# Optimization experiments

Hardware: AMD Instinct MI355X
Metric: run time of the kernel (lower is better)

Reference implementation:

```python
import jax, jax.numpy as jnp
import numpy as np
import math

B, T, H, NH, BLOCK = 2, 2048, 1024, 16, 2048
HS = H // NH  # 64, even as required by RoPE


def make_rope_cache(hs, block):
    # positions t = 1..block (note: source starts at 1, not 0)
    t = np.arange(1, block + 1, dtype=np.float32)[:, None]          # (block, 1)
    i = np.arange(1, hs // 2 + 1, dtype=np.float32)[None, :]        # (1, hs/2)
    theta = (1.0 / 10000.0) ** (2.0 * (i - 1.0) / hs)               # (1, hs/2)
    ang = t * theta                                                  # (block, hs/2)
    return jnp.asarray(np.stack([np.cos(ang), np.sin(ang)], axis=-1))  # (block, hs/2, 2)


def setup_inputs() -> dict:
    key = jax.random.key(0)
    ks = jax.random.split(key, 10)
    s = 0.02
    x = jax.random.normal(ks[0], (B, T, H), jnp.float32)
    masks = jax.random.randint(ks[1], (B, T), 0, 2, jnp.int32)  # 1 = padding token
    Wq = jax.random.normal(ks[2], (H, H), jnp.float32) * s
    bq = jnp.zeros((H,), jnp.float32)
    Wk = jax.random.normal(ks[3], (H, H), jnp.float32) * s
    bk = jnp.zeros((H,), jnp.float32)
    Wv = jax.random.normal(ks[4], (H, H), jnp.float32) * s
    bv = jnp.zeros((H,), jnp.float32)
    Wo = jax.random.normal(ks[5], (H, H), jnp.float32) * s  # final_proj, no bias
    rope = make_rope_cache(HS, BLOCK)
    return {"x": x, "masks": masks, "Wq": Wq, "bq": bq, "Wk": Wk, "bk": bk,
            "Wv": Wv, "bv": bv, "Wo": Wo, "rope": rope}


def _apply_rope(x, cos, sin):
    # x: (B, nh, T, hs); cos/sin: (T, hs/2) broadcast over (B, nh)
    xe, xo = x[..., ::2], x[..., 1::2]
    real = cos * xe - sin * xo
    imag = sin * xe + cos * xo
    return jnp.stack([real, imag], axis=-1).reshape(x.shape)


def reference(x, masks, Wq, bq, Wk, bk, Wv, bv, Wo, rope):
    Bn, Tn, Hn = x.shape
    nh, hs = NH, Hn // NH

    def proj(W, b):
        # torch Linear: x @ W.T + b -> (B, nh, T, hs)
        return (x @ W.T + b).reshape(Bn, Tn, nh, hs).transpose(0, 2, 1, 3)

    Q, K, V = proj(Wq, bq), proj(Wk, bk), proj(Wv, bv)
    cos, sin = rope[:Tn, :, 0], rope[:Tn, :, 1]
    Q = _apply_rope(Q, cos, sin)
    K = _apply_rope(K, cos, sin)

    att = jnp.einsum('bhqd,bhkd->bhqk', Q, K) * (1.0 / math.sqrt(hs))
    causal = jnp.tril(jnp.ones((Tn, Tn), bool))
    att = jnp.where(causal[None, None, :, :], att, -1e10)          # causal mask
    att = jnp.where((masks == 1)[:, None, None, :], -1e10, att)   # padding mask on keys
    att = jax.nn.softmax(att, axis=-1)

    y = jnp.einsum('bhqk,bhkd->bhqd', att, V)
    y = y.transpose(0, 2, 1, 3).reshape(Bn, Tn, Hn)
    return y @ Wo.T  # final_proj has no bias
```

## Files before the change

### kernel.cpp

```cpp
#include <hip/hip_runtime.h>

typedef short short8 __attribute__((ext_vector_type(8)));
typedef float floatx4 __attribute__((ext_vector_type(4)));
typedef unsigned short u16;
typedef unsigned long long u64;

#define Tn 2048
#define Kdim 1024
#define QSCALE 0.18033688011112042f
#define FIXEDMAX 20.0f

__device__ inline u16 f2bf(float x) {
    union { float f; unsigned u; } c; c.f = x;
    unsigned u = c.u;
    u += 0x7fffu + ((u >> 16) & 1u);
    return (u16)(u >> 16);
}
__device__ inline float bf2f(u16 h) {
    union { unsigned u; float f; } c; c.u = ((unsigned)h) << 16;
    return c.f;
}
__device__ inline floatx4 mfma16(short8 a, short8 b, floatx4 c) {
    return __builtin_amdgcn_mfma_f32_16x16x32_bf16(a, b, c, 0, 0, 0);
}
__device__ inline void async16(const void* g, void* l) {
    __builtin_amdgcn_global_load_lds((const __attribute__((address_space(1))) void*)g,
                                     (__attribute__((address_space(3))) void*)l, 16, 0, 0);
}

__global__ __launch_bounds__(256) void cvt_all_k(
    const float* __restrict__ x, const float* __restrict__ wq, const float* __restrict__ wk,
    const float* __restrict__ wv, const float* __restrict__ wo, u16* __restrict__ dst,
    float4* __restrict__ vmz)
{
    int bx = blockIdx.x;
    if (bx >= 8192) {
        int j = threadIdx.x;
        float4 z = {0.f, 0.f, 0.f, 0.f};
        if (j < 512) vmz[j] = z;
        return;
    }
    int i = bx * 256 + threadIdx.x;
    const float* s; int off;
    if (i < 1048576) { s = x; off = i; }
    else {
        int j = i - 1048576; int seg = j >> 18; off = j & 262143;
        s = (seg == 0) ? wq : (seg == 1) ? wk : (seg == 2) ? wv : wo;
    }
    float4 v = ((const float4*)s)[off];
    u64 pk = (u64)f2bf(v.x) | ((u64)f2bf(v.y) << 16) | ((u64)f2bf(v.z) << 32) | ((u64)f2bf(v.w) << 48);
    ((u64*)dst)[i] = pk;
}

__global__ __launch_bounds__(256, 5) void gemm_qkv_k(
    const u16* __restrict__ A,
    const u16* __restrict__ W0, const u16* __restrict__ W1, const u16* __restrict__ W2,
    const float* __restrict__ b0, const float* __restrict__ b1, const float* __restrict__ b2,
    u16* o0, u16* o1, u16* o2,
    const float2* __restrict__ rope, float* __restrict__ vmean)
{
    int bid = blockIdx.x;
    int xcd = bid & 7, bi = bid >> 3;
    int z = bi >> 6;
    int r6 = bi & 63;
    int bx = (xcd & 1) * 8 + (r6 & 7);
    int by = (xcd >> 1) * 8 + (r6 >> 3);

    const u16* W = (z == 0) ? W0 : (z == 1 ? W1 : W2);
    const float* bias = (z == 0) ? b0 : (z == 1 ? b1 : b2);
    u16* outp = (z == 0) ? o0 : (z == 1 ? o1 : o2);

    __shared__ __align__(16) char lds[24576];
    int tid = threadIdx.x;
    int w = tid >> 6, lane = tid & 63, quad = lane >> 4, l15 = lane & 15;
    int m0 = by * 128, n0 = bx * 64;
    int wm = w * 32;

    floatx4 acc[2][4];
    floatx4 vzero = {0.f, 0.f, 0.f, 0.f};
#pragma unroll
    for (int i = 0; i < 2; ++i)
#pragma unroll
        for (int j = 0; j < 4; ++j) acc[i][j] = vzero;

    for (int k0 = 0; k0 < Kdim; k0 += 64) {
#pragma unroll
        for (int j = 0; j < 4; ++j) {
            int f = j * 256 + tid, r = f >> 3, c = (f & 7) ^ (r & 7);
            async16(A + (size_t)(m0 + r) * Kdim + k0 + c * 8, lds + j * 4096 + w * 1024);
        }
#pragma unroll
        for (int j = 0; j < 2; ++j) {
            int f = j * 256 + tid, r = f >> 3, c = (f & 7) ^ (r & 7);
            async16(W + (size_t)(n0 + r) * Kdim + k0 + c * 8, lds + 16384 + j * 4096 + w * 1024);
        }
        __syncthreads();
        short8 af[2][2];
#pragma unroll
        for (int mt = 0; mt < 2; ++mt) {
            int ra = wm + mt * 16 + l15;
            const char* pa = lds + ra * 128;
#pragma unroll
            for (int ks = 0; ks < 2; ++ks)
                af[mt][ks] = *(const short8*)(pa + (((ks * 4 + quad) ^ (ra & 7)) << 4));
        }
#pragma unroll
        for (int ks = 0; ks < 2; ++ks)
#pragma unroll
            for (int nt = 0; nt < 4; ++nt) {
                int rb = nt * 16 + l15;
                short8 bf = *(const short8*)(lds + 16384 + rb * 128 + (((ks * 4 + quad) ^ (rb & 7)) << 4));
                acc[0][nt] = mfma16(af[0][ks], bf, acc[0][nt]);
                acc[1][nt] = mfma16(af[1][ks], bf, acc[1][nt]);
            }
        __syncthreads();
    }

    int mbase = m0 + wm;
    if (z <= 1) {
        float osc = (z == 0) ? QSCALE : 1.0f;
#pragma unroll
        for (int nt = 0; nt < 4; ++nt) {
            int col = n0 + nt * 16 + l15;
            float bv = bias[col];
            int p = (col & 63) >> 1;
#pragma unroll
            for (int mt = 0; mt < 2; ++mt) {
                floatx4 a = acc[mt][nt];
#pragma unroll
                for (int r = 0; r < 4; ++r) {
                    int row = mbase + mt * 16 + quad * 4 + r;
                    float v = a[r] + bv;
                    float ov = __shfl_xor(v, 1, 64);
                    float2 cs = rope[(row & (Tn - 1)) * 32 + p];
                    float res = (cs.x * v + ((lane & 1) ? cs.y * ov : -cs.y * ov)) * osc;
                    float pres = __shfl_xor(res, 1, 64);
                    if (!(lane & 1)) {
                        unsigned pk = (unsigned)f2bf(res) | ((unsigned)f2bf(pres) << 16);
                        *(unsigned*)(outp + (size_t)row * 1024 + col) = pk;
                    }
                }
            }
        }
    } else {
#pragma unroll
        for (int nt = 0; nt < 4; ++nt) {
            int col = n0 + nt * 16 + l15;
            float bv = bias[col];
            float csum = 8.0f * bv;
#pragma unroll
            for (int mt = 0; mt < 2; ++mt) {
                floatx4 a = acc[mt][nt];
                int row0 = mbase + mt * 16 + quad * 4;
                int bb = row0 >> 11, t0 = row0 & (Tn - 1);
                u64 pk = (u64)f2bf(a[0] + bv) | ((u64)f2bf(a[1] + bv) << 16)
                       | ((u64)f2bf(a[2] + bv) << 32) | ((u64)f2bf(a[3] + bv) << 48);
                *(u64*)(outp + (size_t)(bb * 1024 + col) * Tn + t0) = pk;
                csum += a[0] + a[1] + a[2] + a[3];
            }
            csum += __shfl_xor(csum, 16, 64);
            csum += __shfl_xor(csum, 32, 64);
            if (quad == 0) {
                int bb = m0 >> 11;
                atomicAdd(&vmean[bb * 1024 + col], csum);
            }
        }
    }
}

__global__ __launch_bounds__(256, 5) void gemm_o_k(
    const u16* __restrict__ A, const u16* __restrict__ W, float* __restrict__ out)
{
    int bid = blockIdx.x;
    int xcd = bid & 7, bi = bid >> 3;
    int bx = (xcd & 1) * 8 + (bi & 7);
    int by = (xcd >> 1) * 8 + (bi >> 3);

    __shared__ __align__(16) char lds[24576];
    int tid = threadIdx.x;
    int w = tid >> 6, lane = tid & 63, quad = lane >> 4, l15 = lane & 15;
    int m0 = by * 128, n0 = bx * 64;
    int wm = w * 32;

    floatx4 acc[2][4];
    floatx4 vzero = {0.f, 0.f, 0.f, 0.f};
#pragma unroll
    for (int i = 0; i < 2; ++i)
#pragma unroll
        for (int j = 0; j < 4; ++j) acc[i][j] = vzero;

    for (int k0 = 0; k0 < Kdim; k0 += 64) {
#pragma unroll
        for (int j = 0; j < 4; ++j) {
            int f = j * 256 + tid, r = f >> 3, c = (f & 7) ^ (r & 7);
            async16(A + (size_t)(m0 + r) * Kdim + k0 + c * 8, lds + j * 4096 + w * 1024);
        }
#pragma unroll
        for (int j = 0; j < 2; ++j) {
            int f = j * 256 + tid, r = f >> 3, c = (f & 7) ^ (r & 7);
            async16(W + (size_t)(n0 + r) * Kdim + k0 + c * 8, lds + 16384 + j * 4096 + w * 1024);
        }
        __syncthreads();
        short8 af[2][2];
#pragma unroll
        for (int mt = 0; mt < 2; ++mt) {
            int ra = wm + mt * 16 + l15;
            const char* pa = lds + ra * 128;
#pragma unroll
            for (int ks = 0; ks < 2; ++ks)
                af[mt][ks] = *(const short8*)(pa + (((ks * 4 + quad) ^ (ra & 7)) << 4));
        }
#pragma unroll
        for (int ks = 0; ks < 2; ++ks)
#pragma unroll
            for (int nt = 0; nt < 4; ++nt) {
                int rb = nt * 16 + l15;
                short8 bf = *(const short8*)(lds + 16384 + rb * 128 + (((ks * 4 + quad) ^ (rb & 7)) << 4));
                acc[0][nt] = mfma16(af[0][ks], bf, acc[0][nt]);
                acc[1][nt] = mfma16(af[1][ks], bf, acc[1][nt]);
            }
        __syncthreads();
    }

#pragma unroll
    for (int nt = 0; nt < 4; ++nt) {
        int col = n0 + nt * 16 + l15;
#pragma unroll
        for (int mt = 0; mt < 2; ++mt) {
            floatx4 a = acc[mt][nt];
#pragma unroll
            for (int r = 0; r < 4; ++r) {
                int row = m0 + wm + mt * 16 + quad * 4 + r;
                out[(size_t)row * 1024 + col] = a[r];
            }
        }
    }
}

__global__ __launch_bounds__(256) void flash_k(
    const u16* __restrict__ Qb, const u16* __restrict__ Kb, const u16* __restrict__ Vt,
    const int* __restrict__ masks, const float* __restrict__ vmean, u16* __restrict__ Yb)
{
    int bid = blockIdx.x;
    int bh = (bid & 7) * 4 + ((bid >> 3) & 3);
    int idx = bid >> 5;
    int pg = idx >> 3, pr = idx & 7;
    int qt = (pg == 0) ? 31 - pr : (pg == 1) ? pr : (pg == 2) ? 23 - pr : 8 + pr;
    int b = bh >> 4, h = bh & 15;
    int tid = threadIdx.x, w = tid >> 6, lane = tid & 63, quad = lane >> 4, l15 = lane & 15;
    int sc = (lane & 7) ^ (lane >> 3);

    __shared__ __align__(16) u16 ldsK[2][64 * 64];
    __shared__ __align__(16) u16 ldsV[2][64 * 64];
    __shared__ __align__(16) u16 ldsP[4][16 * 64];

    int ktiles = qt + 1;
    unsigned blo = 0, bhi = 0;
    for (int j = 0; j < ktiles; ++j) {
        u64 mk = __ballot(masks[b * Tn + j * 64 + lane] != 0);
        if (lane == j) { blo = (unsigned)mk; bhi = (unsigned)(mk >> 32); }
    }

    auto stage = [&](int bb, int k0) {
#pragma unroll
        for (int j = 0; j < 2; ++j) {
            int row = j * 32 + w * 8 + (lane >> 3);
            const u16* gk = Kb + (size_t)(b * Tn + k0 + row) * 1024 + h * 64 + sc * 8;
            async16(gk, (char*)&ldsK[bb][0] + (j * 32 + w * 8) * 128);
            const u16* gv = Vt + (size_t)(b * 1024 + h * 64 + row) * Tn + k0 + sc * 8;
            async16(gv, (char*)&ldsV[bb][0] + (j * 32 + w * 8) * 128);
        }
    };
    floatx4 vzero = {0.f, 0.f, 0.f, 0.f};

    int q0 = qt * 64 + w * 16;
    short8 qf[2];
    {
        const u16* qp = Qb + (size_t)(b * Tn + q0 + l15) * 1024 + h * 64 + quad * 8;
        qf[0] = *(const short8*)qp;
        qf[1] = *(const short8*)(qp + 32);
    }
    floatx4 o[4];
    float lsum[4] = {0.f, 0.f, 0.f, 0.f};
#pragma unroll
    for (int i = 0; i < 4; ++i) o[i] = vzero;

    stage(0, 0);
    for (int kt = 0; kt < ktiles; ++kt) {
        int k0 = kt * 64;
        int bb = kt & 1;
        __syncthreads();

        short8 kf[4][2], vf[4][2];
#pragma unroll
        for (int f = 0; f < 4; ++f) {
            int key = f * 16 + l15;
            const char* kbase = (const char*)&ldsK[bb][0] + key * 128;
            const char* vbase = (const char*)&ldsV[bb][0] + key * 128;
#pragma unroll
            for (int ks = 0; ks < 2; ++ks) {
                int slot = ((quad + ks * 4) ^ (key & 7)) << 4;
                kf[f][ks] = *(const short8*)(kbase + slot);
                vf[f][ks] = *(const short8*)(vbase + slot);
            }
        }
        if (kt + 1 < ktiles) stage(bb ^ 1, k0 + 64);

        floatx4 s[4];
        __builtin_amdgcn_s_setprio(1);
#pragma unroll
        for (int f = 0; f < 4; ++f) {
            s[f] = mfma16(qf[0], kf[f][0], vzero);
            s[f] = mfma16(qf[1], kf[f][1], s[f]);
        }
        __builtin_amdgcn_s_setprio(0);

        unsigned mlo = __shfl(blo, kt, 64), mhi = __shfl(bhi, kt, 64);
        int mb[4];
        mb[0] = (mlo >> l15) & 1; mb[1] = (mlo >> (l15 + 16)) & 1;
        mb[2] = (mhi >> l15) & 1; mb[3] = (mhi >> (l15 + 16)) & 1;

        if (k0 + 63 <= q0) {
#pragma unroll
            for (int r = 0; r < 4; ++r) {
                float psum = 0.f;
#pragma unroll
                for (int f = 0; f < 4; ++f) {
                    float v = mb[f] ? -1e10f : s[f][r];
                    float p = __builtin_amdgcn_exp2f(v - FIXEDMAX);
                    psum += p;
                    unsigned u = __float_as_uint(p) + 0x8000u;
                    int row = quad * 4 + r, key = f * 16 + l15;
                    *((u16*)((char*)&ldsP[w][0] + row * 128 +
                             ((((key >> 3) ^ (row & 7))) << 4) + (key & 7) * 2)) = (u16)(u >> 16);
                }
                lsum[r] += psum;
            }
        } else {
#pragma unroll
            for (int r = 0; r < 4; ++r) {
                int lim = q0 + quad * 4 + r - k0;
                float psum = 0.f;
#pragma unroll
                for (int f = 0; f < 4; ++f) {
                    float v = (16 * f + l15 > lim || mb[f]) ? -1e10f : s[f][r];
                    float p = __builtin_amdgcn_exp2f(v - FIXEDMAX);
                    psum += p;
                    unsigned u = __float_as_uint(p) + 0x8000u;
                    int row = quad * 4 + r, key = f * 16 + l15;
                    *((u16*)((char*)&ldsP[w][0] + row * 128 +
                             ((((key >> 3) ^ (row & 7))) << 4) + (key & 7) * 2)) = (u16)(u >> 16);
                }
                lsum[r] += psum;
            }
        }
        __asm__ volatile("s_waitcnt lgkmcnt(0)" ::: "memory");
        short8 pf0 = *(const short8*)((const char*)&ldsP[w][0] + l15 * 128 + ((quad ^ (l15 & 7)) << 4));
        short8 pf1 = *(const short8*)((const char*)&ldsP[w][0] + l15 * 128 + (((quad + 4) ^ (l15 & 7)) << 4));
        __builtin_amdgcn_s_setprio(1);
#pragma unroll
        for (int nb = 0; nb < 4; ++nb) {
            o[nb] = mfma16(pf0, vf[nb][0], o[nb]);
            o[nb] = mfma16(pf1, vf[nb][1], o[nb]);
        }
        __builtin_amdgcn_s_setprio(0);
    }

#pragma unroll
    for (int r = 0; r < 4; ++r) {
        int qq = q0 + quad * 4 + r;
        float l = lsum[r];
#pragma unroll
        for (int off = 1; off < 16; off <<= 1) l += __shfl_xor(l, off, 64);
        bool degen = (l == 0.f);
        float linv = 1.0f / l;
#pragma unroll
        for (int nb = 0; nb < 4; ++nb) {
            int d = nb * 16 + l15;
            float val = degen ? vmean[b * 1024 + h * 64 + d] * (1.f / 2048.f) : o[nb][r] * linv;
            float pv = __shfl_xor(val, 1, 64);
            if (!(lane & 1)) {
                unsigned pk = (unsigned)f2bf(val) | ((unsigned)f2bf(pv) << 16);
                *(unsigned*)(Yb + (size_t)(b * Tn + qq) * 1024 + h * 64 + d) = pk;
            }
        }
    }
}

extern "C" void kernel_launch(void* const* d_in, const int* in_sizes, int n_in,
                              void* d_out, int out_size, void* d_ws, size_t ws_size,
                              hipStream_t stream) {
    const float* x  = (const float*)d_in[0];
    const int* masks = (const int*)d_in[1];
    const float* Wq = (const float*)d_in[2];
    const float* bq = (const float*)d_in[3];
    const float* Wk = (const float*)d_in[4];
    const float* bk = (const float*)d_in[5];
    const float* Wv = (const float*)d_in[6];
    const float* bv = (const float*)d_in[7];
    const float* Wo = (const float*)d_in[8];
    const float2* rope = (const float2*)d_in[9];
    float* out = (float*)d_out;

    char* ws = (char*)d_ws;
    u16* xb   = (u16*)(ws);
    u16* Wqb  = (u16*)(ws + (8  << 20));
    u16* Wkb  = (u16*)(ws + (10 << 20));
    u16* Wvb  = (u16*)(ws + (12 << 20));
    u16* Wob  = (u16*)(ws + (14 << 20));
    u16* Qb   = (u16*)(ws + (16 << 20));
    u16* Kb2  = (u16*)(ws + (24 << 20));
    u16* Vt   = (u16*)(ws + (32 << 20));
    u16* Yb   = (u16*)(ws + (40 << 20));
    float* vm = (float*)(ws + (48 << 20));

    cvt_all_k<<<8193, 256, 0, stream>>>(x, Wq, Wk, Wv, Wo, xb, (float4*)vm);

    gemm_qkv_k<<<1536, 256, 0, stream>>>(xb, Wqb, Wkb, Wvb, bq, bk, bv,
                                         Qb, Kb2, Vt, rope, vm);
    flash_k<<<1024, 256, 0, stream>>>(Qb, Kb2, Vt, masks, vm, Yb);
    gemm_o_k<<<512, 256, 0, stream>>>(Yb, Wob, out);
}
```

Before: 189.9 us.

## Compact non-padded keys/values so flash attention skips masked key tiles

Adds a prefix-sum kernel over the padding mask and scatters K and V rows into a compacted layout that holds only unmasked tokens, so flash attention iterates only over as many key tiles as there are valid keys up to the query tile. The combined causal/padding mask becomes a per-element comparison against the query's prefix count, folded into the MFMA accumulator init, and the per-tile ballot bitmask setup is removed. In exchange it adds an extra kernel launch, zeroing of the compacted K buffer, and scattered, uncoalesced V-transpose writes in the projection epilogue. With roughly half the tokens padded, the attention work should drop substantially.

```diff
diff --git a/kernel.cpp b/kernel.cpp
--- a/kernel.cpp
+++ b/kernel.cpp
@@ -31,13 +31,18 @@
 __global__ __launch_bounds__(256) void cvt_all_k(
     const float* __restrict__ x, const float* __restrict__ wq, const float* __restrict__ wk,
     const float* __restrict__ wv, const float* __restrict__ wo, u16* __restrict__ dst,
-    float4* __restrict__ vmz)
+    float4* __restrict__ vmz, float4* __restrict__ kvz)
 {
     int bx = blockIdx.x;
     if (bx >= 8192) {
-        int j = threadIdx.x;
+        int e = bx - 8192;
         float4 z = {0.f, 0.f, 0.f, 0.f};
-        if (j < 512) vmz[j] = z;
+        if (e == 0) {
+            vmz[threadIdx.x] = z;
+            vmz[threadIdx.x + 256] = z;
+        } else {
+            kvz[(e - 1) * 256 + threadIdx.x] = z;
+        }
         return;
     }
     int i = bx * 256 + threadIdx.x;
@@ -52,12 +57,31 @@
     ((u64*)dst)[i] = pk;
 }
 
+__global__ __launch_bounds__(1024) void compact_k(const int* __restrict__ masks, int* __restrict__ prefQ) {
+    int b = blockIdx.x, t = threadIdx.x;
+    __shared__ int tmp[1024];
+    int v0 = (masks[b * Tn + 2 * t] == 0);
+    int v1 = (masks[b * Tn + 2 * t + 1] == 0);
+    tmp[t] = v0 + v1;
+    __syncthreads();
+    for (int off = 1; off < 1024; off <<= 1) {
+        int v = (t >= off) ? tmp[t - off] : 0;
+        __syncthreads();
+        tmp[t] += v;
+        __syncthreads();
+    }
+    int incl = tmp[t];
+    prefQ[b * Tn + 2 * t] = incl - v1;
+    prefQ[b * Tn + 2 * t + 1] = incl;
+}
+
 __global__ __launch_bounds__(256, 5) void gemm_qkv_k(
     const u16* __restrict__ A,
     const u16* __restrict__ W0, const u16* __restrict__ W1, const u16* __restrict__ W2,
     const float* __restrict__ b0, const float* __restrict__ b1, const float* __restrict__ b2,
     u16* o0, u16* o1, u16* o2,
-    const float2* __restrict__ rope, float* __restrict__ vmean)
+    const float2* __restrict__ rope, float* __restrict__ vmean,
+    const int* __restrict__ masks, const int* __restrict__ prefQ)
 {
     int bid = blockIdx.x;
     int xcd = bid & 7, bi = bid >> 3;
@@ -68,7 +92,6 @@
 
     const u16* W = (z == 0) ? W0 : (z == 1 ? W1 : W2);
     const float* bias = (z == 0) ? b0 : (z == 1 ? b1 : b2);
-    u16* outp = (z == 0) ? o0 : (z == 1 ? o1 : o2);
 
     __shared__ __align__(16) char lds[24576];
     int tid = threadIdx.x;
@@ -127,9 +150,18 @@
 #pragma unroll
             for (int mt = 0; mt < 2; ++mt) {
                 floatx4 a = acc[mt][nt];
+                int row0 = mbase + mt * 16 + quad * 4;
+                int bb2 = row0 >> 11, tt0 = row0 & (Tn - 1);
+                int mka[4] = {0, 0, 0, 0}, pqa[4] = {0, 0, 0, 0};
+                if (z == 1) {
+                    int4 mk = *(const int4*)(masks + bb2 * Tn + tt0);
+                    int4 pq = *(const int4*)(prefQ + bb2 * Tn + tt0);
+                    mka[0] = mk.x; mka[1] = mk.y; mka[2] = mk.z; mka[3] = mk.w;
+                    pqa[0] = pq.x; pqa[1] = pq.y; pqa[2] = pq.z; pqa[3] = pq.w;
+                }
 #pragma unroll
                 for (int r = 0; r < 4; ++r) {
-                    int row = mbase + mt * 16 + quad * 4 + r;
+                    int row = row0 + r;
                     float v = a[r] + bv;
                     float ov = __shfl_xor(v, 1, 64);
                     float2 cs = rope[(row & (Tn - 1)) * 32 + p];
@@ -137,7 +169,12 @@
                     float pres = __shfl_xor(res, 1, 64);
                     if (!(lane & 1)) {
                         unsigned pk = (unsigned)f2bf(res) | ((unsigned)f2bf(pres) << 16);
-                        *(unsigned*)(outp + (size_t)row * 1024 + col) = pk;
+                        if (z == 0) {
+                            *(unsigned*)(o0 + (size_t)row * 1024 + col) = pk;
+                        } else if (mka[r] == 0) {
+                            int rowc = bb2 * Tn + pqa[r] - 1;
+                            *(unsigned*)(o1 + (size_t)rowc * 1024 + col) = pk;
+                        }
                     }
                 }
             }
@@ -152,10 +189,16 @@
             for (int mt = 0; mt < 2; ++mt) {
                 floatx4 a = acc[mt][nt];
                 int row0 = mbase + mt * 16 + quad * 4;
-                int bb = row0 >> 11, t0 = row0 & (Tn - 1);
-                u64 pk = (u64)f2bf(a[0] + bv) | ((u64)f2bf(a[1] + bv) << 16)
-                       | ((u64)f2bf(a[2] + bv) << 32) | ((u64)f2bf(a[3] + bv) << 48);
-                *(u64*)(outp + (size_t)(bb * 1024 + col) * Tn + t0) = pk;
+                int bb2 = row0 >> 11, t0 = row0 & (Tn - 1);
+                int4 mk = *(const int4*)(masks + bb2 * Tn + t0);
+                int4 pq = *(const int4*)(prefQ + bb2 * Tn + t0);
+                int mka[4] = {mk.x, mk.y, mk.z, mk.w};
+                int pqa[4] = {pq.x, pq.y, pq.z, pq.w};
+#pragma unroll
+                for (int i = 0; i < 4; ++i) {
+                    if (mka[i] == 0)
+                        o2[(size_t)(bb2 * 1024 + col) * Tn + pqa[i] - 1] = f2bf(a[i] + bv);
+                }
                 csum += a[0] + a[1] + a[2] + a[3];
             }
             csum += __shfl_xor(csum, 16, 64);
@@ -238,8 +281,8 @@
 }
 
 __global__ __launch_bounds__(256) void flash_k(
-    const u16* __restrict__ Qb, const u16* __restrict__ Kb, const u16* __restrict__ Vt,
-    const int* __restrict__ masks, const float* __restrict__ vmean, u16* __restrict__ Yb)
+    const u16* __restrict__ Qb, const u16* __restrict__ Kc, const u16* __restrict__ Vtc,
+    const int* __restrict__ prefQ, const float* __restrict__ vmean, u16* __restrict__ Yb)
 {
     int bid = blockIdx.x;
     int bh = (bid & 7) * 4 + ((bid >> 3) & 3);
@@ -254,26 +297,25 @@
     __shared__ __align__(16) u16 ldsV[2][64 * 64];
     __shared__ __align__(16) u16 ldsP[4][16 * 64];
 
-    int ktiles = qt + 1;
-    unsigned blo = 0, bhi = 0;
-    for (int j = 0; j < ktiles; ++j) {
-        u64 mk = __ballot(masks[b * Tn + j * 64 + lane] != 0);
-        if (lane == j) { blo = (unsigned)mk; bhi = (unsigned)(mk >> 32); }
-    }
+    int ktiles = (prefQ[b * Tn + qt * 64 + 63] + 63) >> 6;
 
     auto stage = [&](int bb, int k0) {
 #pragma unroll
         for (int j = 0; j < 2; ++j) {
             int row = j * 32 + w * 8 + (lane >> 3);
-            const u16* gk = Kb + (size_t)(b * Tn + k0 + row) * 1024 + h * 64 + sc * 8;
+            const u16* gk = Kc + (size_t)(b * Tn + k0 + row) * 1024 + h * 64 + sc * 8;
             async16(gk, (char*)&ldsK[bb][0] + (j * 32 + w * 8) * 128);
-            const u16* gv = Vt + (size_t)(b * 1024 + h * 64 + row) * Tn + k0 + sc * 8;
+            const u16* gv = Vtc + (size_t)(b * 1024 + h * 64 + row) * Tn + k0 + sc * 8;
             async16(gv, (char*)&ldsV[bb][0] + (j * 32 + w * 8) * 128);
         }
     };
     floatx4 vzero = {0.f, 0.f, 0.f, 0.f};
 
     int q0 = qt * 64 + w * 16;
+    int pq[4];
+#pragma unroll
+    for (int r = 0; r < 4; ++r) pq[r] = prefQ[b * Tn + q0 + quad * 4 + r];
+
     short8 qf[2];
     {
         const u16* qp = Qb + (size_t)(b * Tn + q0 + l15) * 1024 + h * 64 + quad * 8;
@@ -285,7 +327,7 @@
 #pragma unroll
     for (int i = 0; i < 4; ++i) o[i] = vzero;
 
-    stage(0, 0);
+    if (ktiles > 0) stage(0, 0);
     for (int kt = 0; kt < ktiles; ++kt) {
         int k0 = kt * 64;
         int bb = kt & 1;
@@ -306,53 +348,37 @@
         }
         if (kt + 1 < ktiles) stage(bb ^ 1, k0 + 64);
 
+        floatx4 ci[4];
+#pragma unroll
+        for (int f = 0; f < 4; ++f) {
+            int jj = k0 + f * 16 + l15;
+#pragma unroll
+            for (int r = 0; r < 4; ++r)
+                ci[f][r] = (jj < pq[r]) ? -FIXEDMAX : -1e10f;
+        }
+
         floatx4 s[4];
         __builtin_amdgcn_s_setprio(1);
 #pragma unroll
         for (int f = 0; f < 4; ++f) {
-            s[f] = mfma16(qf[0], kf[f][0], vzero);
+            s[f] = mfma16(qf[0], kf[f][0], ci[f]);
             s[f] = mfma16(qf[1], kf[f][1], s[f]);
         }
         __builtin_amdgcn_s_setprio(0);
 
-        unsigned mlo = __shfl(blo, kt, 64), mhi = __shfl(bhi, kt, 64);
-        int mb[4];
-        mb[0] = (mlo >> l15) & 1; mb[1] = (mlo >> (l15 + 16)) & 1;
-        mb[2] = (mhi >> l15) & 1; mb[3] = (mhi >> (l15 + 16)) & 1;
-
-        if (k0 + 63 <= q0) {
-#pragma unroll
-            for (int r = 0; r < 4; ++r) {
-                float psum = 0.f;
-#pragma unroll
-                for (int f = 0; f < 4; ++f) {
-                    float v = mb[f] ? -1e10f : s[f][r];
-                    float p = __builtin_amdgcn_exp2f(v - FIXEDMAX);
-                    psum += p;
-                    unsigned u = __float_as_uint(p) + 0x8000u;
-                    int row = quad * 4 + r, key = f * 16 + l15;
-                    *((u16*)((char*)&ldsP[w][0] + row * 128 +
-                             ((((key >> 3) ^ (row & 7))) << 4) + (key & 7) * 2)) = (u16)(u >> 16);
-                }
-                lsum[r] += psum;
-            }
-        } else {
-#pragma unroll
-            for (int r = 0; r < 4; ++r) {
-                int lim = q0 + quad * 4 + r - k0;
-                float psum = 0.f;
-#pragma unroll
-                for (int f = 0; f < 4; ++f) {
-                    float v = (16 * f + l15 > lim || mb[f]) ? -1e10f : s[f][r];
-                    float p = __builtin_amdgcn_exp2f(v - FIXEDMAX);
-                    psum += p;
-                    unsigned u = __float_as_uint(p) + 0x8000u;
-                    int row = quad * 4 + r, key = f * 16 + l15;
-                    *((u16*)((char*)&ldsP[w][0] + row * 128 +
-                             ((((key >> 3) ^ (row & 7))) << 4) + (key & 7) * 2)) = (u16)(u >> 16);
-                }
-                lsum[r] += psum;
-            }
+#pragma unroll
+        for (int r = 0; r < 4; ++r) {
+            float psum = 0.f;
+#pragma unroll
+            for (int f = 0; f < 4; ++f) {
+                float p = __builtin_amdgcn_exp2f(s[f][r]);
+                psum += p;
+                unsigned u = __float_as_uint(p) + 0x8000u;
+                int row = quad * 4 + r, key = f * 16 + l15;
+                *((u16*)((char*)&ldsP[w][0] + row * 128 +
+                         ((((key >> 3) ^ (row & 7))) << 4) + (key & 7) * 2)) = (u16)(u >> 16);
+            }
+            lsum[r] += psum;
         }
         __asm__ volatile("s_waitcnt lgkmcnt(0)" ::: "memory");
         short8 pf0 = *(const short8*)((const char*)&ldsP[w][0] + l15 * 128 + ((quad ^ (l15 & 7)) << 4));
@@ -413,11 +439,16 @@
     u16* Vt   = (u16*)(ws + (32 << 20));
     u16* Yb   = (u16*)(ws + (40 << 20));
     float* vm = (float*)(ws + (48 << 20));
-
-    cvt_all_k<<<8193, 256, 0, stream>>>(x, Wq, Wk, Wv, Wo, xb, (float4*)vm);
+    int* prefQ = (int*)(ws + (48 << 20) + 32768);
+
+    cvt_all_k<<<12289, 256, 0, stream>>>(x, Wq, Wk, Wv, Wo, xb, (float4*)vm, (float4*)Kb2);
+
+    compact_k<<<2, 1024, 0, stream>>>(masks, prefQ);
 
     gemm_qkv_k<<<1536, 256, 0, stream>>>(xb, Wqb, Wkb, Wvb, bq, bk, bv,
-                                         Qb, Kb2, Vt, rope, vm);
-    flash_k<<<1024, 256, 0, stream>>>(Qb, Kb2, Vt, masks, vm, Yb);
+                                         Qb, Kb2, Vt, rope, vm, masks, prefQ);
+
+    flash_k<<<1024, 256, 0, stream>>>(Qb, Kb2, Vt, prefQ, vm, Yb);
+
     gemm_o_k<<<512, 256, 0, stream>>>(Yb, Wob, out);
 }
```

Result: no change. 187.3 us (-1.4%).
